# Optimization experiments

Measured on AMD Instinct MI355X. Metric: run time of the kernel, lower is better.

The kernel has to match this reference:

```python
import jax, jax.numpy as jnp
import numpy as np

B, SQ, SK, D = 8, 4096, 4096, 64


def setup_inputs() -> dict:
    key = jax.random.key(0)
    k1, k2, k3 = jax.random.split(key, 3)
    x1 = jax.random.normal(k1, (B, SQ, D), dtype=jnp.float32)   # queries
    x2 = jax.random.normal(k2, (B, SK, D), dtype=jnp.float32)   # keys
    x3 = jax.random.normal(k3, (B, SK, D), dtype=jnp.float32)   # values
    x4 = 0                                                      # dropout p (static, 0 => deterministic)
    x5 = jnp.ones((1,), dtype=jnp.float32)                      # scale divisor
    return {"x1": x1, "x2": x2, "x3": x3, "x4": x4, "x5": x5}


def reference(x1, x2, x3, x4, x5):
    # scores: [B, Sq, Sk]
    scores = jnp.einsum("bqd,bkd->bqk", x1, x2) / x5
    attn = jax.nn.softmax(scores, axis=-1)
    p = float(x4)  # static python scalar
    if p > 0.0:
        mask = jax.random.bernoulli(jax.random.key(42), 1.0 - p, attn.shape)
        attn = attn * mask.astype(attn.dtype) / (1.0 - p)
    # out: [B, Sq, D]
    return jnp.einsum("bqk,bkd->bqd", attn, x3)
```

## Files before the change

kernel.cpp:

```cpp
#include <hip/hip_runtime.h>


typedef _Float16 f16x8 __attribute__((ext_vector_type(8)));
typedef _Float16 f16x4 __attribute__((ext_vector_type(4)));
typedef __fp16   h16x2 __attribute__((ext_vector_type(2)));
typedef float    f32x4 __attribute__((ext_vector_type(4)));

constexpr int kB  = 8;
constexpr int kSQ = 4096;
constexpr int kSK = 4096;
constexpr int kD  = 64;
constexpr int KSPLIT = 4;
constexpr int SKH = kSK / KSPLIT;
constexpr int BQ  = 128;
constexpr int BK  = 64;
constexpr int LDP = BK + 8;
constexpr size_t APART = (size_t)kB * kSQ * kD;

static __device__ __forceinline__ f16x4 pack4(float a, float b, float c, float d) {
    h16x2 p0 = __builtin_amdgcn_cvt_pkrtz(a, b);
    h16x2 p1 = __builtin_amdgcn_cvt_pkrtz(c, d);
    f16x4 r;
    r[0] = (_Float16)p0[0]; r[1] = (_Float16)p0[1];
    r[2] = (_Float16)p1[0]; r[3] = (_Float16)p1[1];
    return r;
}
static __device__ __forceinline__ f16x8 pack8(const float4& a, const float4& c) {
    f16x4 lo = pack4(a.x, a.y, a.z, a.w);
    f16x4 hi = pack4(c.x, c.y, c.z, c.w);
    f16x8 f;
    f[0] = lo[0]; f[1] = lo[1]; f[2] = lo[2]; f[3] = lo[3];
    f[4] = hi[0]; f[5] = hi[1]; f[6] = hi[2]; f[7] = hi[3];
    return f;
}

typedef const __attribute__((address_space(1))) unsigned int* gu32p;
typedef __attribute__((address_space(3))) unsigned int* lu32p;
static __device__ __forceinline__ void gload_lds16(const void* g, void* l) {
    __builtin_amdgcn_global_load_lds((gu32p)g, (lu32p)l, 16, 0, 0);
}

__global__ __launch_bounds__(256, 2)
void fattn_prepass(const float* __restrict__ Kg,
                   const float* __restrict__ Vg,
                   _Float16* __restrict__ Kh,
                   _Float16* __restrict__ Vt)
{
    __shared__ _Float16 tr[kD][BK];

    const int tid = threadIdx.x;
    const int kt  = blockIdx.x;
    const int b   = blockIdx.y;

    const int k = tid >> 2;
    const int p = tid & 3;
    const int gk = kt * BK + k;

    {
        const float* src = Kg + ((size_t)b * kSK + gk) * kD + p * 16;
        const float4 a0 = *(const float4*)(src + 0);
        const float4 a1 = *(const float4*)(src + 4);
        const float4 a2 = *(const float4*)(src + 8);
        const float4 a3 = *(const float4*)(src + 12);
        _Float16* dst = Kh + ((size_t)b * kSK + gk) * kD;
        const int fb0 = 2 * p, fb1 = 2 * p + 1;
        *(f16x8*)&dst[(fb0 ^ (gk & 7)) * 8] = pack8(a0, a1);
        *(f16x8*)&dst[(fb1 ^ (gk & 7)) * 8] = pack8(a2, a3);
    }

    {
        const float* src = Vg + ((size_t)b * kSK + gk) * kD + p * 16;
        const float4 a0 = *(const float4*)(src + 0);
        const float4 a1 = *(const float4*)(src + 4);
        const float4 a2 = *(const float4*)(src + 8);
        const float4 a3 = *(const float4*)(src + 12);
        const float v[16] = {a0.x,a0.y,a0.z,a0.w, a1.x,a1.y,a1.z,a1.w,
                             a2.x,a2.y,a2.z,a2.w, a3.x,a3.y,a3.z,a3.w};
#pragma unroll
        for (int j = 0; j < 16; ++j)
            tr[p * 16 + j][k] = (_Float16)v[j];
    }
    __syncthreads();
    {
        const int f  = tid >> 2;
        const int p2 = tid & 3;
        const f16x8 b0 = *(const f16x8*)&tr[f][p2 * 16 + 0];
        const f16x8 b1 = *(const f16x8*)&tr[f][p2 * 16 + 8];
        _Float16* dst = Vt + (((size_t)b * 64 + kt) * kD + f) * BK;
        const int kb0 = 2 * p2, kb1 = 2 * p2 + 1;
        *(f16x8*)&dst[(kb0 ^ (f & 7)) * 8] = b0;
        *(f16x8*)&dst[(kb1 ^ (f & 7)) * 8] = b1;
    }
}

__global__ __launch_bounds__(256, 3)
void fattn_partial(const float* __restrict__ Qg,
                   const _Float16* __restrict__ Kh,
                   const _Float16* __restrict__ Vt,
                   const float* __restrict__ sdiv,
                   _Float16* __restrict__ Ap,
                   float2* __restrict__ MLp)
{
    __shared__ __align__(16) _Float16 sK[2][BK * kD];
    __shared__ __align__(16) _Float16 sV[2][kD * BK];
    __shared__ __align__(16) _Float16 sP[4][2][16][LDP];

    const int tid  = threadIdx.x;
    const int w    = tid >> 6;
    const int lane = tid & 63;
    const int l16  = lane & 15;
    const int quad = lane >> 4;
    const int sw   = (quad ^ (l16 & 7)) * 8;

    const int b  = blockIdx.y;
    const int qb = blockIdx.x * BQ;
    const int ks = blockIdx.z;

    const float inv_scale = 1.0f / sdiv[0];

    const float* Qb = Qg + ((size_t)b * kSQ + qb) * kD;
    const _Float16* Khb = Kh + ((size_t)b * kSK + (size_t)ks * SKH) * kD;
    const _Float16* Vtb = Vt + (((size_t)b * 64 + (size_t)ks * (SKH / BK)) * kD) * BK;

    f16x8 qf[2][2];
#pragma unroll
    for (int mt = 0; mt < 2; ++mt) {
        const float* qrow = Qb + (size_t)(w * 32 + mt * 16 + l16) * kD;
#pragma unroll
        for (int kk = 0; kk < 2; ++kk) {
            const float4 a = *(const float4*)(qrow + kk * 32 + quad * 8);
            const float4 c = *(const float4*)(qrow + kk * 32 + quad * 8 + 4);
            float4 as = make_float4(a.x * inv_scale, a.y * inv_scale, a.z * inv_scale, a.w * inv_scale);
            float4 cs = make_float4(c.x * inv_scale, c.y * inv_scale, c.z * inv_scale, c.w * inv_scale);
            qf[mt][kk] = pack8(as, cs);
        }
    }

    auto stage = [&](int kt, int buf) {
        const char* gk = (const char*)(Khb + (size_t)kt * BK * kD) + w * 2048 + lane * 16;
        const char* gv = (const char*)(Vtb + (size_t)kt * kD * BK) + w * 2048 + lane * 16;
        char* lk = (char*)&sK[buf][0] + w * 2048;
        char* lv = (char*)&sV[buf][0] + w * 2048;
        gload_lds16(gk,        lk);
        gload_lds16(gk + 1024, lk + 1024);
        gload_lds16(gv,        lv);
        gload_lds16(gv + 1024, lv + 1024);
    };

    f32x4 o[2][4];
    float m_i[2] = {-1e30f, -1e30f}, l_i[2] = {0.0f, 0.0f};
#pragma unroll
    for (int mt = 0; mt < 2; ++mt)
#pragma unroll
        for (int dt = 0; dt < 4; ++dt)
#pragma unroll
            for (int r = 0; r < 4; ++r) o[mt][dt][r] = 0.0f;

    stage(0, 0);
    __syncthreads();

    const int nIter = SKH / BK;
    for (int kt = 0; kt < nIter; ++kt) {
        const int buf = kt & 1;
        const bool more = (kt + 1 < nIter);
        if (more) stage(kt + 1, buf ^ 1);

        f32x4 s[2][4];
#pragma unroll
        for (int nt = 0; nt < 4; ++nt) {
            const int krow = (nt * 16 + l16) * kD;
            const f16x8 kf0 = *(const f16x8*)&sK[buf][krow + sw];
            const f16x8 kf1 = *(const f16x8*)&sK[buf][krow + (sw ^ 32)];
#pragma unroll
            for (int mt = 0; mt < 2; ++mt) {
                f32x4 acc;
#pragma unroll
                for (int r = 0; r < 4; ++r) acc[r] = 0.0f;
                acc = __builtin_amdgcn_mfma_f32_16x16x32_f16(kf0, qf[mt][0], acc, 0, 0, 0);
                acc = __builtin_amdgcn_mfma_f32_16x16x32_f16(kf1, qf[mt][1], acc, 0, 0, 0);
                s[mt][nt] = acc;
            }
        }

#pragma unroll
        for (int mt = 0; mt < 2; ++mt) {
            float rm = s[mt][0][0];
#pragma unroll
            for (int nt = 0; nt < 4; ++nt)
#pragma unroll
                for (int r = 0; r < 4; ++r) rm = fmaxf(rm, s[mt][nt][r]);
            rm = fmaxf(rm, __shfl_xor(rm, 16, 64));
            rm = fmaxf(rm, __shfl_xor(rm, 32, 64));
            const float mnew = fmaxf(m_i[mt], rm);
            const float alpha = __expf(m_i[mt] - mnew);
            m_i[mt] = mnew;
            float rs = 0.0f;
#pragma unroll
            for (int nt = 0; nt < 4; ++nt)
#pragma unroll
                for (int r = 0; r < 4; ++r) {
                    const float p = __expf(s[mt][nt][r] - mnew);
                    s[mt][nt][r] = p;
                    rs += p;
                }
            rs += __shfl_xor(rs, 16, 64);
            rs += __shfl_xor(rs, 32, 64);
            l_i[mt] = l_i[mt] * alpha + rs;
#pragma unroll
            for (int dt = 0; dt < 4; ++dt)
#pragma unroll
                for (int r = 0; r < 4; ++r) o[mt][dt][r] *= alpha;
#pragma unroll
            for (int nt = 0; nt < 4; ++nt)
                *(f16x4*)&sP[w][mt][l16][nt * 16 + quad * 4] =
                    pack4(s[mt][nt][0], s[mt][nt][1], s[mt][nt][2], s[mt][nt][3]);
        }

        const f16x8 pfa0 = *(const f16x8*)&sP[w][0][l16][quad * 8];
        const f16x8 pfa1 = *(const f16x8*)&sP[w][0][l16][32 + quad * 8];
        const f16x8 pfb0 = *(const f16x8*)&sP[w][1][l16][quad * 8];
        const f16x8 pfb1 = *(const f16x8*)&sP[w][1][l16][32 + quad * 8];
#pragma unroll
        for (int dt = 0; dt < 4; ++dt) {
            const int frow = (dt * 16 + l16) * BK;
            const f16x8 vf0 = *(const f16x8*)&sV[buf][frow + sw];
            const f16x8 vf1 = *(const f16x8*)&sV[buf][frow + (sw ^ 32)];
            o[0][dt] = __builtin_amdgcn_mfma_f32_16x16x32_f16(vf0, pfa0, o[0][dt], 0, 0, 0);
            o[0][dt] = __builtin_amdgcn_mfma_f32_16x16x32_f16(vf1, pfa1, o[0][dt], 0, 0, 0);
            o[1][dt] = __builtin_amdgcn_mfma_f32_16x16x32_f16(vf0, pfb0, o[1][dt], 0, 0, 0);
            o[1][dt] = __builtin_amdgcn_mfma_f32_16x16x32_f16(vf1, pfb1, o[1][dt], 0, 0, 0);
        }

        __syncthreads();
    }

    _Float16* Ab = Ap + (size_t)ks * APART + ((size_t)b * kSQ + qb) * kD;
    float2* MLb = MLp + (size_t)ks * kB * kSQ + (size_t)b * kSQ + qb;
#pragma unroll
    for (int mt = 0; mt < 2; ++mt) {
        const int row = w * 32 + mt * 16 + l16;
#pragma unroll
        for (int dt = 0; dt < 4; ++dt)
            *(f16x4*)&Ab[(size_t)row * kD + dt * 16 + quad * 4] =
                pack4(o[mt][dt][0], o[mt][dt][1], o[mt][dt][2], o[mt][dt][3]);
        if (quad == 0) MLb[row] = make_float2(m_i[mt], l_i[mt]);
    }
}

__global__ __launch_bounds__(256)
void fattn_combine(const _Float16* __restrict__ Ap,
                   const float2* __restrict__ MLp,
                   float* __restrict__ Og)
{
    const int idx = blockIdx.x * 256 + threadIdx.x;
    const int r = idx >> 4;
    const int c = (idx & 15) * 4;

    float m = -1e30f;
    float2 ml[KSPLIT];
#pragma unroll
    for (int s = 0; s < KSPLIT; ++s) {
        ml[s] = MLp[(size_t)s * kB * kSQ + r];
        m = fmaxf(m, ml[s].x);
    }
    float acc[4] = {0.f, 0.f, 0.f, 0.f};
    float lsum = 0.f;
#pragma unroll
    for (int s = 0; s < KSPLIT; ++s) {
        const float e = __expf(ml[s].x - m);
        lsum += e * ml[s].y;
        const f16x4 a = *(const f16x4*)&Ap[(size_t)s * APART + (size_t)r * kD + c];
#pragma unroll
        for (int j = 0; j < 4; ++j) acc[j] += e * (float)a[j];
    }
    const float inv = 1.0f / lsum;
    float4 res = make_float4(acc[0] * inv, acc[1] * inv, acc[2] * inv, acc[3] * inv);
    *(float4*)&Og[(size_t)r * kD + c] = res;
}

extern "C" void kernel_launch(void* const* d_in, const int* in_sizes, int n_in,
                              void* d_out, int out_size, void* d_ws, size_t ws_size,
                              hipStream_t stream) {
    const float* Q    = (const float*)d_in[0];
    const float* K    = (const float*)d_in[1];
    const float* V    = (const float*)d_in[2];
    const float* sdiv = (const float*)d_in[4];
    float* O = (float*)d_out;

    _Float16* Kh  = (_Float16*)d_ws;
    _Float16* Vt  = Kh + (size_t)kB * kSK * kD;
    _Float16* Ap  = Vt + (size_t)kB * kSK * kD;
    float2*   MLp = (float2*)(Ap + (size_t)KSPLIT * APART);

    fattn_prepass<<<dim3(kSK / BK, kB), dim3(256), 0, stream>>>(K, V, Kh, Vt);
    dim3 grid(kSQ / BQ, kB, KSPLIT);
    fattn_partial<<<grid, dim3(256), 0, stream>>>(Q, Kh, Vt, sdiv, Ap, MLp);
    fattn_combine<<<dim3(kB * kSQ * kD / (256 * 4)), dim3(256), 0, stream>>>(Ap, MLp, O);
}
```

Before: 146.7 us.

## Load K/V fragments directly from global memory, drop LDS staging and barriers

Removes the double-buffered LDS staging of K and V tiles and the per-iteration block barrier. Each wave now reads its MFMA fragments straight from global memory (relying on the pre-swizzled fp16 layout and the cache). LDS use drops to the P buffer, so occupancy is raised to 4 blocks per SM. The online-softmax rescale is also skipped when no row max changed across the wave. The cost is that each wave fetches K/V independently and global load latency is no longer hidden by prefetching.

```diff
diff --git a/kernel.cpp b/kernel.cpp
--- a/kernel.cpp
+++ b/kernel.cpp
@@ -34,12 +34,6 @@
     return f;
 }
 
-typedef const __attribute__((address_space(1))) unsigned int* gu32p;
-typedef __attribute__((address_space(3))) unsigned int* lu32p;
-static __device__ __forceinline__ void gload_lds16(const void* g, void* l) {
-    __builtin_amdgcn_global_load_lds((gu32p)g, (lu32p)l, 16, 0, 0);
-}
-
 __global__ __launch_bounds__(256, 2)
 void fattn_prepass(const float* __restrict__ Kg,
                    const float* __restrict__ Vg,
@@ -93,7 +87,7 @@
     }
 }
 
-__global__ __launch_bounds__(256, 3)
+__global__ __launch_bounds__(256, 4)
 void fattn_partial(const float* __restrict__ Qg,
                    const _Float16* __restrict__ Kh,
                    const _Float16* __restrict__ Vt,
@@ -101,8 +95,6 @@
                    _Float16* __restrict__ Ap,
                    float2* __restrict__ MLp)
 {
-    __shared__ __align__(16) _Float16 sK[2][BK * kD];
-    __shared__ __align__(16) _Float16 sV[2][kD * BK];
     __shared__ __align__(16) _Float16 sP[4][2][16][LDP];
 
     const int tid  = threadIdx.x;
@@ -119,8 +111,8 @@
     const float inv_scale = 1.0f / sdiv[0];
 
     const float* Qb = Qg + ((size_t)b * kSQ + qb) * kD;
-    const _Float16* Khb = Kh + ((size_t)b * kSK + (size_t)ks * SKH) * kD;
-    const _Float16* Vtb = Vt + (((size_t)b * 64 + (size_t)ks * (SKH / BK)) * kD) * BK;
+    const _Float16* Kt = Kh + ((size_t)b * kSK + (size_t)ks * SKH) * kD;
+    const _Float16* Vtt = Vt + (((size_t)b * 64 + (size_t)ks * (SKH / BK)) * kD) * BK;
 
     f16x8 qf[2][2];
 #pragma unroll
@@ -136,17 +128,6 @@
         }
     }
 
-    auto stage = [&](int kt, int buf) {
-        const char* gk = (const char*)(Khb + (size_t)kt * BK * kD) + w * 2048 + lane * 16;
-        const char* gv = (const char*)(Vtb + (size_t)kt * kD * BK) + w * 2048 + lane * 16;
-        char* lk = (char*)&sK[buf][0] + w * 2048;
-        char* lv = (char*)&sV[buf][0] + w * 2048;
-        gload_lds16(gk,        lk);
-        gload_lds16(gk + 1024, lk + 1024);
-        gload_lds16(gv,        lv);
-        gload_lds16(gv + 1024, lv + 1024);
-    };
-
     f32x4 o[2][4];
     float m_i[2] = {-1e30f, -1e30f}, l_i[2] = {0.0f, 0.0f};
 #pragma unroll
@@ -156,30 +137,38 @@
 #pragma unroll
             for (int r = 0; r < 4; ++r) o[mt][dt][r] = 0.0f;
 
-    stage(0, 0);
-    __syncthreads();
-
     const int nIter = SKH / BK;
     for (int kt = 0; kt < nIter; ++kt) {
-        const int buf = kt & 1;
-        const bool more = (kt + 1 < nIter);
-        if (more) stage(kt + 1, buf ^ 1);
-
-        f32x4 s[2][4];
+        const _Float16* Kb2 = Kt  + (size_t)kt * BK * kD;
+        const _Float16* Vb2 = Vtt + (size_t)kt * kD * BK;
+
+        f16x8 kf[4][2];
 #pragma unroll
         for (int nt = 0; nt < 4; ++nt) {
             const int krow = (nt * 16 + l16) * kD;
-            const f16x8 kf0 = *(const f16x8*)&sK[buf][krow + sw];
-            const f16x8 kf1 = *(const f16x8*)&sK[buf][krow + (sw ^ 32)];
+            kf[nt][0] = *(const f16x8*)&Kb2[krow + sw];
+            kf[nt][1] = *(const f16x8*)&Kb2[krow + (sw ^ 32)];
+        }
+
+        f32x4 s[2][4];
+#pragma unroll
+        for (int nt = 0; nt < 4; ++nt)
 #pragma unroll
             for (int mt = 0; mt < 2; ++mt) {
                 f32x4 acc;
 #pragma unroll
                 for (int r = 0; r < 4; ++r) acc[r] = 0.0f;
-                acc = __builtin_amdgcn_mfma_f32_16x16x32_f16(kf0, qf[mt][0], acc, 0, 0, 0);
-                acc = __builtin_amdgcn_mfma_f32_16x16x32_f16(kf1, qf[mt][1], acc, 0, 0, 0);
+                acc = __builtin_amdgcn_mfma_f32_16x16x32_f16(kf[nt][0], qf[mt][0], acc, 0, 0, 0);
+                acc = __builtin_amdgcn_mfma_f32_16x16x32_f16(kf[nt][1], qf[mt][1], acc, 0, 0, 0);
                 s[mt][nt] = acc;
             }
+
+        f16x8 vf[4][2];
+#pragma unroll
+        for (int dt = 0; dt < 4; ++dt) {
+            const int frow = (dt * 16 + l16) * BK;
+            vf[dt][0] = *(const f16x8*)&Vb2[frow + sw];
+            vf[dt][1] = *(const f16x8*)&Vb2[frow + (sw ^ 32)];
         }
 
 #pragma unroll
@@ -192,8 +181,6 @@
             rm = fmaxf(rm, __shfl_xor(rm, 16, 64));
             rm = fmaxf(rm, __shfl_xor(rm, 32, 64));
             const float mnew = fmaxf(m_i[mt], rm);
-            const float alpha = __expf(m_i[mt] - mnew);
-            m_i[mt] = mnew;
             float rs = 0.0f;
 #pragma unroll
             for (int nt = 0; nt < 4; ++nt)
@@ -205,11 +192,16 @@
                 }
             rs += __shfl_xor(rs, 16, 64);
             rs += __shfl_xor(rs, 32, 64);
-            l_i[mt] = l_i[mt] * alpha + rs;
-#pragma unroll
-            for (int dt = 0; dt < 4; ++dt)
-#pragma unroll
-                for (int r = 0; r < 4; ++r) o[mt][dt][r] *= alpha;
+            if (!__all(mnew == m_i[mt])) {
+                const float alpha = __expf(m_i[mt] - mnew);
+                l_i[mt] *= alpha;
+#pragma unroll
+                for (int dt = 0; dt < 4; ++dt)
+#pragma unroll
+                    for (int r = 0; r < 4; ++r) o[mt][dt][r] *= alpha;
+            }
+            m_i[mt] = mnew;
+            l_i[mt] += rs;
 #pragma unroll
             for (int nt = 0; nt < 4; ++nt)
                 *(f16x4*)&sP[w][mt][l16][nt * 16 + quad * 4] =
@@ -222,16 +214,11 @@
         const f16x8 pfb1 = *(const f16x8*)&sP[w][1][l16][32 + quad * 8];
 #pragma unroll
         for (int dt = 0; dt < 4; ++dt) {
-            const int frow = (dt * 16 + l16) * BK;
-            const f16x8 vf0 = *(const f16x8*)&sV[buf][frow + sw];
-            const f16x8 vf1 = *(const f16x8*)&sV[buf][frow + (sw ^ 32)];
-            o[0][dt] = __builtin_amdgcn_mfma_f32_16x16x32_f16(vf0, pfa0, o[0][dt], 0, 0, 0);
-            o[0][dt] = __builtin_amdgcn_mfma_f32_16x16x32_f16(vf1, pfa1, o[0][dt], 0, 0, 0);
-            o[1][dt] = __builtin_amdgcn_mfma_f32_16x16x32_f16(vf0, pfb0, o[1][dt], 0, 0, 0);
-            o[1][dt] = __builtin_amdgcn_mfma_f32_16x16x32_f16(vf1, pfb1, o[1][dt], 0, 0, 0);
-        }
-
-        __syncthreads();
+            o[0][dt] = __builtin_amdgcn_mfma_f32_16x16x32_f16(vf[dt][0], pfa0, o[0][dt], 0, 0, 0);
+            o[0][dt] = __builtin_amdgcn_mfma_f32_16x16x32_f16(vf[dt][1], pfa1, o[0][dt], 0, 0, 0);
+            o[1][dt] = __builtin_amdgcn_mfma_f32_16x16x32_f16(vf[dt][0], pfb0, o[1][dt], 0, 0, 0);
+            o[1][dt] = __builtin_amdgcn_mfma_f32_16x16x32_f16(vf[dt][1], pfb1, o[1][dt], 0, 0, 0);
+        }
     }
 
     _Float16* Ab = Ap + (size_t)ks * APART + ((size_t)b * kSQ + qb) * kD;
```

After: 188.9 us. +28.8%, slower.
